# Kernel optimization log

Measured on AMD Instinct MI355X. Metric: run time of the kernel, lower is better.

Reference implementation:

```python
import jax, jax.numpy as jnp
import numpy as np

N_EMBED = 1024
HEAD_SIZE = 64


def setup_inputs() -> dict:
    key = jax.random.key(0)
    kx, kq, kk, kv = jax.random.split(key, 4)
    x = jax.random.normal(kx, (8, 2048, N_EMBED), dtype=jnp.float32)
    s = 1.0 / np.sqrt(N_EMBED)
    # nn.Linear weights are [out, in]; store as [in, out] for x @ W
    W_q = jax.random.uniform(kq, (N_EMBED, HEAD_SIZE), jnp.float32, -s, s)
    W_k = jax.random.uniform(kk, (N_EMBED, HEAD_SIZE), jnp.float32, -s, s)
    W_v = jax.random.uniform(kv, (N_EMBED, HEAD_SIZE), jnp.float32, -s, s)
    return {"x": x, "W_q": W_q, "W_k": W_k, "W_v": W_v}


def reference(x, W_q, W_k, W_v):
    b, t, c = x.shape
    q = x @ W_q  # [b, t, h]
    k = x @ W_k
    v = x @ W_v
    scale = k.shape[-1] ** -0.5
    wei = jnp.einsum("bqh,bkh->bqk", q, k) * scale  # [b, t, t]
    causal = jnp.tril(jnp.ones((t, t), dtype=bool))
    wei = jnp.where(causal, wei, -jnp.inf)
    wei = jax.nn.softmax(wei, axis=-1)
    # dropout p=0.0 -> identity
    return jnp.einsum("bqk,bkh->bqh", wei, v)
```

## Files before the change

kernel.cpp:

```cpp
#include <hip/hip_runtime.h>
#include <math.h>

typedef unsigned short u16;
typedef unsigned int u32;
typedef __attribute__((ext_vector_type(4))) float f32x4;
typedef __attribute__((ext_vector_type(8))) short s16x8;
typedef __attribute__((ext_vector_type(4))) unsigned short u16x4;

#define T_ 2048
#define C_ 1024

__device__ __forceinline__ u16 f2b(float f) {
  u32 u = __builtin_bit_cast(u32, f);
  return (u16)((u + 0x8000u) >> 16);
}

__device__ __forceinline__ s16x8 pack8v(f32x4 a, f32x4 b) {
  s16x8 r;
  r[0] = (short)f2b(a[0]); r[1] = (short)f2b(a[1]);
  r[2] = (short)f2b(a[2]); r[3] = (short)f2b(a[3]);
  r[4] = (short)f2b(b[0]); r[5] = (short)f2b(b[1]);
  r[6] = (short)f2b(b[2]); r[7] = (short)f2b(b[3]);
  return r;
}

__device__ __forceinline__ void gld_lds16(const void* g, void* l) {
  __builtin_amdgcn_global_load_lds(
      (const __attribute__((address_space(1))) u32*)g,
      (__attribute__((address_space(3))) u32*)l, 16, 0, 0);
}

__global__ __launch_bounds__(256) void wconv(const float* __restrict__ Wq,
                                             const float* __restrict__ Wk,
                                             const float* __restrict__ Wv,
                                             u16* __restrict__ Wt) {
  __shared__ u16 t[64][68];
  const int bm = blockIdx.x >> 4;
  const int kt = blockIdx.x & 15;
  const float* src = (bm == 0) ? Wq : ((bm == 1) ? Wk : Wv);
  const float scale = (bm == 0) ? 0.18033688f : 1.0f;
  const int krow = threadIdx.x >> 2;
  const int c0 = (threadIdx.x & 3) * 16;
  const float* sp = src + (size_t)(kt * 64 + krow) * 64 + c0;
#pragma unroll
  for (int i = 0; i < 4; ++i) {
    float4 v = *(const float4*)(sp + i * 4);
    t[c0 + i * 4 + 0][krow] = f2b(v.x * scale);
    t[c0 + i * 4 + 1][krow] = f2b(v.y * scale);
    t[c0 + i * 4 + 2][krow] = f2b(v.z * scale);
    t[c0 + i * 4 + 3][krow] = f2b(v.w * scale);
  }
  __syncthreads();
  const int n = threadIdx.x >> 2;
  const int koff = (threadIdx.x & 3) * 16;
  u16* dst = Wt + (size_t)(bm * 64 + n) * C_ + kt * 64 + koff;
#pragma unroll
  for (int i = 0; i < 4; ++i)
    *(u16x4*)(dst + i * 4) = *(const u16x4*)(&t[n][koff + i * 4]);
}

__global__ __launch_bounds__(256, 2) void proj(const float* __restrict__ x,
                                               const u16* __restrict__ Wt,
                                               u16* __restrict__ qo,
                                               u16* __restrict__ ko,
                                               u16* __restrict__ vt) {
  __shared__ __align__(16) u32 smem[16384];
  float* xs = (float*)smem;
  u16* wsh = (u16*)(smem + 4096);
  const int tid = threadIdx.x;
  const int wave = tid >> 6, lane = tid & 63;
  const int quad = lane >> 4, l15 = lane & 15;
  const int mg = wave >> 1, nh = wave & 1;
  const int m0 = blockIdx.x * 32;

  const int xslot = lane & 31, xrin = lane >> 5;
  const int wslot = lane & 15, wrin = lane >> 4;

  f32x4 acc[6];
#pragma unroll
  for (int j = 0; j < 6; ++j) acc[j] = {0.f, 0.f, 0.f, 0.f};

  for (int kt = 0; kt < 8; ++kt) {
    const int k0 = kt * 128;
#pragma unroll
    for (int c = 0; c < 4; ++c) {
      const int row = wave * 8 + c * 2 + xrin;
      const int g = xslot ^ (row & 31);
      gld_lds16(x + (size_t)(m0 + row) * C_ + k0 + g * 4,
                &xs[(wave * 8 + c * 2) * 128]);
    }
#pragma unroll
    for (int c = 0; c < 12; ++c) {
      const int row = (wave * 12 + c) * 4 + wrin;
      const int g = wslot ^ (row & 15);
      gld_lds16(Wt + (size_t)row * C_ + k0 + g * 8,
                &wsh[(wave * 12 + c) * 4 * 128]);
    }
    __syncthreads();
    const int r = 16 * mg + l15;
    s16x8 af[4];
#pragma unroll
    for (int ks = 0; ks < 4; ++ks) {
      const int cc = ks * 8 + quad * 2;
      f32x4 p0 = *(const f32x4*)&xs[r * 128 + ((cc ^ (r & 31)) * 4)];
      f32x4 p1 = *(const f32x4*)&xs[r * 128 + (((cc + 1) ^ (r & 31)) * 4)];
      af[ks] = pack8v(p0, p1);
    }
#pragma unroll
    for (int jj = 0; jj < 6; ++jj) {
      const int R = (nh * 6 + jj) * 16 + l15;
#pragma unroll
      for (int ks = 0; ks < 4; ++ks) {
        const int cc = ks * 4 + quad;
        s16x8 bf = *(const s16x8*)&wsh[R * 128 + ((cc ^ (R & 15)) * 8)];
        acc[jj] = __builtin_amdgcn_mfma_f32_16x16x32_bf16(af[ks], bf, acc[jj], 0, 0, 0);
      }
    }
    __syncthreads();
  }

  const int r0 = m0 + 16 * mg + quad * 4;
#pragma unroll
  for (int jj = 0; jj < 6; ++jj) {
    const int ns = nh * 6 + jj;
    if (ns < 4) {
      const int col = ns * 16 + l15;
#pragma unroll
      for (int i = 0; i < 4; ++i)
        qo[(size_t)(r0 + i) * 64 + col] = f2b(acc[jj][i]);
    } else if (ns < 8) {
      const int col = (ns - 4) * 16 + l15;
#pragma unroll
      for (int i = 0; i < 4; ++i)
        ko[(size_t)(r0 + i) * 64 + col] = f2b(acc[jj][i]);
    } else {
      const int d = (ns - 8) * 16 + l15;
      const int bb = r0 >> 11, t0 = r0 & 2047;
      u16x4 pk = {f2b(acc[jj][0]), f2b(acc[jj][1]), f2b(acc[jj][2]), f2b(acc[jj][3])};
      *(u16x4*)(vt + (size_t)bb * (64 * T_) + (size_t)d * T_ + t0) = pk;
    }
  }
}

__global__ __launch_bounds__(256, 2) void attn(const u16* __restrict__ qw,
                                               const u16* __restrict__ kw,
                                               const u16* __restrict__ vt,
                                               float* __restrict__ out) {
  __shared__ __align__(16) u16 kvb[2][2][2][4096];
  __shared__ __align__(16) u16 Ob[4][16 * 72];
  __shared__ float mbuf[4][16];
  __shared__ float lbuf[4][16];
  const int tid = threadIdx.x;
  const int wave = tid >> 6, lane = tid & 63;
  const int quad = lane >> 4, l15 = lane & 15;
  const int qg = wave >> 1, kg = wave & 1;
  const int b = blockIdx.x & 7;
  const int qt = 63 - (blockIdx.x >> 3);

  const u16* qp = qw + ((size_t)b * T_ + qt * 32 + 16 * qg) * 64;
  const u16* kb = kw + (size_t)b * T_ * 64;
  const u16* vb = vt + (size_t)b * 64 * T_;

  const int jd = qt >> 1;
  const int R = (jd + 2) >> 1;

  s16x8 qf[2];
#pragma unroll
  for (int ks = 0; ks < 2; ++ks)
    qf[ks] = *(const s16x8*)(qp + l15 * 64 + ks * 32 + quad * 8);

  f32x4 o[4];
#pragma unroll
  for (int m = 0; m < 4; ++m) o[m] = {0.f, 0.f, 0.f, 0.f};
  float mr = -INFINITY, lr = 0.0f;

  u16* P = Ob[wave];

  const int rin = lane >> 3, slot = lane & 7;
  const int g8 = slot ^ rin;

  auto stage = [&](int r) {
    const int j = 2 * r + (wave >> 1);
    if (j > jd) return;
    u16* dst = kvb[r & 1][wave >> 1][wave & 1];
    if ((wave & 1) == 0) {
#pragma unroll
      for (int c = 0; c < 8; ++c)
        gld_lds16(kb + (size_t)(64 * j + 8 * c + rin) * 64 + g8 * 8,
                  dst + c * 512);
    } else {
#pragma unroll
      for (int c = 0; c < 8; ++c)
        gld_lds16(vb + (size_t)(8 * c + rin) * T_ + 64 * j + g8 * 8,
                  dst + c * 512);
    }
  };

  stage(0);
  __syncthreads();

  for (int r = 0; r < R; ++r) {
    if (r + 1 < R) stage(r + 1);
    const int j = 2 * r + kg;
    if (j <= jd) {
      const u16* Kt = kvb[r & 1][kg][0];
      const u16* Vt = kvb[r & 1][kg][1];
      f32x4 s[4];
#pragma unroll
      for (int m = 0; m < 4; ++m) s[m] = {0.f, 0.f, 0.f, 0.f};
#pragma unroll
      for (int ks = 0; ks < 2; ++ks)
#pragma unroll
        for (int m = 0; m < 4; ++m) {
          const int row = 16 * m + l15;
          const int sl = (ks * 4 + quad) ^ (row & 7);
          s16x8 kf = *(const s16x8*)&Kt[row * 64 + sl * 8];
          s[m] = __builtin_amdgcn_mfma_f32_16x16x32_bf16(kf, qf[ks], s[m], 0, 0, 0);
        }
      if (j == jd) {
#pragma unroll
        for (int m = 0; m < 4; ++m)
#pragma unroll
          for (int i = 0; i < 4; ++i)
            if (64 * jd + 16 * m + quad * 4 + i > 32 * qt + 16 * qg + l15)
              s[m][i] = -INFINITY;
      }
      float mt = s[0][0];
#pragma unroll
      for (int m = 0; m < 4; ++m)
#pragma unroll
        for (int i = 0; i < 4; ++i) mt = fmaxf(mt, s[m][i]);
      mt = fmaxf(mt, __shfl_xor(mt, 16));
      mt = fmaxf(mt, __shfl_xor(mt, 32));
      const float mn = fmaxf(mr, mt);
      const float al = exp2f(mr - mn);
      mr = mn;
      float rs = 0.0f;
#pragma unroll
      for (int m = 0; m < 4; ++m)
#pragma unroll
        for (int i = 0; i < 4; ++i) {
          float p = exp2f(s[m][i] - mn);
          s[m][i] = p;
          rs += p;
        }
      rs += __shfl_xor(rs, 16);
      rs += __shfl_xor(rs, 32);
      lr = lr * al + rs;
#pragma unroll
      for (int m = 0; m < 4; ++m) {
        u16x4 pk = {f2b(s[m][0]), f2b(s[m][1]), f2b(s[m][2]), f2b(s[m][3])};
        *(u16x4*)(&P[l15 * 72 + 16 * m + quad * 4]) = pk;
      }
#pragma unroll
      for (int m = 0; m < 4; ++m) o[m] *= al;
#pragma unroll
      for (int ks = 0; ks < 2; ++ks) {
        s16x8 pf = *(const s16x8*)(&P[l15 * 72 + ks * 32 + quad * 8]);
#pragma unroll
        for (int m = 0; m < 4; ++m) {
          const int row = 16 * m + l15;
          const int sl = (ks * 4 + quad) ^ (row & 7);
          s16x8 vf = *(const s16x8*)&Vt[row * 64 + sl * 8];
          o[m] = __builtin_amdgcn_mfma_f32_16x16x32_bf16(vf, pf, o[m], 0, 0, 0);
        }
      }
    }
    __syncthreads();
  }

  if (quad == 0) {
    mbuf[wave][l15] = mr;
    lbuf[wave][l15] = lr;
  }
#pragma unroll
  for (int m = 0; m < 4; ++m) {
    u16x4 pk = {f2b(o[m][0]), f2b(o[m][1]), f2b(o[m][2]), f2b(o[m][3])};
    *(u16x4*)(&Ob[wave][l15 * 72 + 16 * m + quad * 4]) = pk;
  }
  __syncthreads();
  const int rr = tid >> 3;
  const int cg = (tid & 7) * 8;
  const int qgr = rr >> 4, r16 = rr & 15;
  const float m0 = mbuf[qgr * 2][r16], m1 = mbuf[qgr * 2 + 1][r16];
  const float mstar = fmaxf(m0, m1);
  const float f0 = exp2f(m0 - mstar), f1 = exp2f(m1 - mstar);
  const float lsum = f0 * lbuf[qgr * 2][r16] + f1 * lbuf[qgr * 2 + 1][r16];
  const float inv = 1.0f / lsum;
  s16x8 o0 = *(const s16x8*)(&Ob[qgr * 2][r16 * 72 + cg]);
  s16x8 o1 = *(const s16x8*)(&Ob[qgr * 2 + 1][r16 * 72 + cg]);
  float av[8];
#pragma unroll
  for (int e = 0; e < 8; ++e) {
    float x0 = __builtin_bit_cast(float, ((u32)(u16)o0[e]) << 16);
    float x1 = __builtin_bit_cast(float, ((u32)(u16)o1[e]) << 16);
    av[e] = (f0 * x0 + f1 * x1) * inv;
  }
  float* op = out + ((size_t)b * T_ + qt * 32 + rr) * 64 + cg;
  float4 st0 = {av[0], av[1], av[2], av[3]};
  float4 st1 = {av[4], av[5], av[6], av[7]};
  *(float4*)(op + 0) = st0;
  *(float4*)(op + 4) = st1;
}

extern "C" void kernel_launch(void* const* d_in, const int* in_sizes, int n_in,
                              void* d_out, int out_size, void* d_ws, size_t ws_size,
                              hipStream_t stream) {
  const float* x  = (const float*)d_in[0];
  const float* Wq = (const float*)d_in[1];
  const float* Wk = (const float*)d_in[2];
  const float* Wv = (const float*)d_in[3];
  float* out = (float*)d_out;
  char* ws = (char*)d_ws;
  u16* Wt = (u16*)ws;
  u16* q  = (u16*)(ws + 393216);
  u16* k  = (u16*)(ws + 393216 + 2097152);
  u16* vT = (u16*)(ws + 393216 + 2 * 2097152);
  hipLaunchKernelGGL(wconv, dim3(48), dim3(256), 0, stream, Wq, Wk, Wv, Wt);
  hipLaunchKernelGGL(proj, dim3(512), dim3(256), 0, stream, x, Wt, q, k, vT);
  hipLaunchKernelGGL(attn, dim3(512), dim3(256), 0, stream, q, k, vT, out);
}
```

Before: 132.0 us.

## Double-buffer projection GEMM with bf16 x staging in LDS and 64-row tiles

The projection kernel now works on 64-row tiles with 512 threads and double-buffers both the weight and activation tiles in LDS. The next K-slice is prefetched while the current one is multiplied. Activations are converted to bf16 in registers before being stored to LDS, which halves LDS traffic compared with staging fp32 and packing after the read. The trade-off is more LDS use, a larger block, and K steps of 64 with more barriers.

```diff
diff --git a/kernel.cpp b/kernel.cpp
--- a/kernel.cpp
+++ b/kernel.cpp
@@ -15,12 +15,12 @@
   return (u16)((u + 0x8000u) >> 16);
 }
 
-__device__ __forceinline__ s16x8 pack8v(f32x4 a, f32x4 b) {
+__device__ __forceinline__ s16x8 pack8(float4 a, float4 b) {
   s16x8 r;
-  r[0] = (short)f2b(a[0]); r[1] = (short)f2b(a[1]);
-  r[2] = (short)f2b(a[2]); r[3] = (short)f2b(a[3]);
-  r[4] = (short)f2b(b[0]); r[5] = (short)f2b(b[1]);
-  r[6] = (short)f2b(b[2]); r[7] = (short)f2b(b[3]);
+  r[0] = (short)f2b(a.x); r[1] = (short)f2b(a.y);
+  r[2] = (short)f2b(a.z); r[3] = (short)f2b(a.w);
+  r[4] = (short)f2b(b.x); r[5] = (short)f2b(b.y);
+  r[6] = (short)f2b(b.z); r[7] = (short)f2b(b.w);
   return r;
 }
 
@@ -59,63 +59,75 @@
     *(u16x4*)(dst + i * 4) = *(const u16x4*)(&t[n][koff + i * 4]);
 }
 
-__global__ __launch_bounds__(256, 2) void proj(const float* __restrict__ x,
+__global__ __launch_bounds__(512, 2) void proj(const float* __restrict__ x,
                                                const u16* __restrict__ Wt,
                                                u16* __restrict__ qo,
                                                u16* __restrict__ ko,
                                                u16* __restrict__ vt) {
-  __shared__ __align__(16) u32 smem[16384];
-  float* xs = (float*)smem;
-  u16* wsh = (u16*)(smem + 4096);
+  __shared__ __align__(16) u16 xs[2][64 * 64];
+  __shared__ __align__(16) u16 wsh[2][192 * 64];
   const int tid = threadIdx.x;
   const int wave = tid >> 6, lane = tid & 63;
   const int quad = lane >> 4, l15 = lane & 15;
   const int mg = wave >> 1, nh = wave & 1;
-  const int m0 = blockIdx.x * 32;
-
-  const int xslot = lane & 31, xrin = lane >> 5;
-  const int wslot = lane & 15, wrin = lane >> 4;
+  const int m0 = blockIdx.x * 64;
+
+  const int rin = lane >> 3, slot = lane & 7;
+  const int xrow = tid >> 3, xcg = (tid & 7) * 8;
+  const float* xp = x + (size_t)(m0 + xrow) * C_ + xcg;
+  const int xslot = (tid & 7) ^ (xrow & 7);
+
+  auto stageW = [&](int kt, int buf) {
+#pragma unroll
+    for (int c = 0; c < 3; ++c) {
+      const int row0 = 24 * wave + 8 * c;
+      const int g = slot ^ rin;
+      gld_lds16(Wt + (size_t)(row0 + rin) * C_ + kt * 64 + g * 8,
+                &wsh[buf][row0 * 64]);
+    }
+  };
 
   f32x4 acc[6];
 #pragma unroll
   for (int j = 0; j < 6; ++j) acc[j] = {0.f, 0.f, 0.f, 0.f};
 
-  for (int kt = 0; kt < 8; ++kt) {
-    const int k0 = kt * 128;
-#pragma unroll
-    for (int c = 0; c < 4; ++c) {
-      const int row = wave * 8 + c * 2 + xrin;
-      const int g = xslot ^ (row & 31);
-      gld_lds16(x + (size_t)(m0 + row) * C_ + k0 + g * 4,
-                &xs[(wave * 8 + c * 2) * 128]);
-    }
-#pragma unroll
-    for (int c = 0; c < 12; ++c) {
-      const int row = (wave * 12 + c) * 4 + wrin;
-      const int g = wslot ^ (row & 15);
-      gld_lds16(Wt + (size_t)row * C_ + k0 + g * 8,
-                &wsh[(wave * 12 + c) * 4 * 128]);
-    }
-    __syncthreads();
-    const int r = 16 * mg + l15;
-    s16x8 af[4];
-#pragma unroll
-    for (int ks = 0; ks < 4; ++ks) {
-      const int cc = ks * 8 + quad * 2;
-      f32x4 p0 = *(const f32x4*)&xs[r * 128 + ((cc ^ (r & 31)) * 4)];
-      f32x4 p1 = *(const f32x4*)&xs[r * 128 + (((cc + 1) ^ (r & 31)) * 4)];
-      af[ks] = pack8v(p0, p1);
+  stageW(0, 0);
+  {
+    float4 p0 = *(const float4*)(xp);
+    float4 p1 = *(const float4*)(xp + 4);
+    *(s16x8*)(&xs[0][xrow * 64 + xslot * 8]) = pack8(p0, p1);
+  }
+  __syncthreads();
+
+  for (int kt = 0; kt < 16; ++kt) {
+    const int buf = kt & 1;
+    float4 p0, p1;
+    if (kt < 15) {
+      stageW(kt + 1, buf ^ 1);
+      p0 = *(const float4*)(xp + (kt + 1) * 64);
+      p1 = *(const float4*)(xp + (kt + 1) * 64 + 4);
+    }
+    s16x8 af[2];
+    {
+      const int r = 16 * mg + l15;
+#pragma unroll
+      for (int ks = 0; ks < 2; ++ks) {
+        const int sl = (ks * 4 + quad) ^ (l15 & 7);
+        af[ks] = *(const s16x8*)&xs[buf][r * 64 + sl * 8];
+      }
     }
 #pragma unroll
     for (int jj = 0; jj < 6; ++jj) {
       const int R = (nh * 6 + jj) * 16 + l15;
 #pragma unroll
-      for (int ks = 0; ks < 4; ++ks) {
-        const int cc = ks * 4 + quad;
-        s16x8 bf = *(const s16x8*)&wsh[R * 128 + ((cc ^ (R & 15)) * 8)];
+      for (int ks = 0; ks < 2; ++ks) {
+        const int sl = (ks * 4 + quad) ^ (l15 & 7);
+        s16x8 bf = *(const s16x8*)&wsh[buf][R * 64 + sl * 8];
         acc[jj] = __builtin_amdgcn_mfma_f32_16x16x32_bf16(af[ks], bf, acc[jj], 0, 0, 0);
       }
     }
+    if (kt < 15)
+      *(s16x8*)(&xs[buf ^ 1][xrow * 64 + xslot * 8]) = pack8(p0, p1);
     __syncthreads();
   }
 
@@ -314,9 +326,9 @@
   char* ws = (char*)d_ws;
   u16* Wt = (u16*)ws;
   u16* q  = (u16*)(ws + 393216);
-  u16* k  = (u16*)(ws + 393216 + 2097152);
-  u16* vT = (u16*)(ws + 393216 + 2 * 2097152);
+  u16* k  = (u16*)(ws + 2490368);
+  u16* vT = (u16*)(ws + 4587520);
   hipLaunchKernelGGL(wconv, dim3(48), dim3(256), 0, stream, Wq, Wk, Wv, Wt);
-  hipLaunchKernelGGL(proj, dim3(512), dim3(256), 0, stream, x, Wt, q, k, vT);
+  hipLaunchKernelGGL(proj, dim3(256), dim3(512), 0, stream, x, Wt, q, k, vT);
   hipLaunchKernelGGL(attn, dim3(512), dim3(256), 0, stream, q, k, vT, out);
 }
```

Measured after the change: 137.5 us. +4.2%, slower.
